# Kernel tuning notes

Hardware: AMD Instinct MI355X
Metric: run time of the kernel (lower is better)

The kernel has to match this reference:

```python
import jax, jax.numpy as jnp
import numpy as np

NUM_HEADS = 8
HEAD_DIM = 64
D_MODEL = NUM_HEADS * HEAD_DIM  # 512
B, T = 4, 2048


def setup_inputs() -> dict:
    key = jax.random.key(0)
    k1, k2 = jax.random.split(key)
    x = jax.random.normal(k1, (B, T, D_MODEL), dtype=jnp.float32)
    mask = jnp.ones((B, 1, T, T), dtype=jnp.float32)
    W = jax.random.normal(k2, (D_MODEL, 3 * D_MODEL), dtype=jnp.float32) * (D_MODEL ** -0.5)
    b = jnp.zeros((3 * D_MODEL,), dtype=jnp.float32)
    return {"x": x, "mask": mask, "W": W, "b": b}


def reference(x, mask, W, b):
    batch = x.shape[0]
    # fused QKV projection: [B, T, 3D]
    qkv = jnp.einsum("btd,de->bte", x, W) + b
    # NOTE: faithful to torch reshape [B, T, H, Hd, 3] -> the size-3 axis is innermost
    qkv = qkv.reshape(batch, -1, NUM_HEADS, HEAD_DIM, 3)
    qkv = jnp.transpose(qkv, (4, 0, 2, 1, 3))  # [3, B, H, T, Hd]
    q, k, v = qkv[0], qkv[1], qkv[2]
    logits = jnp.einsum("bhqd,bhkd->bhqk", q, k) / (HEAD_DIM ** 0.5)
    logits = logits + (1.0 - mask) * -10000.0
    w = jax.nn.softmax(logits, axis=-1)
    out = jnp.einsum("bhqk,bhkd->bhqd", w, v)  # [B, H, T, Hd]
    out = jnp.transpose(out, (0, 2, 1, 3)).reshape(batch, -1, NUM_HEADS * HEAD_DIM)
    return out
```

## Files before the change

kernel.cpp:

```cpp
#include <hip/hip_runtime.h>
#include <hip/hip_bf16.h>
#include <stdint.h>

#define B_   4
#define T_   2048
#define H_   8
#define HD_  64
#define DM_  512
#define N3_  1536

typedef short bf_el;
typedef __attribute__((ext_vector_type(8))) bf_el bfrag;
typedef __attribute__((ext_vector_type(4))) bf_el bhalf4;
typedef __attribute__((ext_vector_type(4))) float ffrag;

#define SCALE_L2E  0.18033688011112043f
#define MASK_L2E   14426.950408889634f

static __device__ __forceinline__ unsigned short f2bf(float f) {
    union { float f; unsigned int i; } v; v.f = f;
    unsigned int r = v.i + 0x7fff + ((v.i >> 16) & 1);
    return (unsigned short)(r >> 16);
}
static __device__ __forceinline__ unsigned short f2bf_fast(float f) {
    union { float f; unsigned int i; } v; v.f = f;
    return (unsigned short)((v.i + 0x8000u) >> 16);
}

static __device__ __forceinline__ unsigned int cvt_pk_bf16(float a, float b) {
    unsigned int r;
    asm("v_cvt_pk_bf16_f32 %0, %1, %2" : "=v"(r) : "v"(a), "v"(b));
    return r;
}

__global__ __launch_bounds__(256) void k_prep(const float* __restrict__ W,
                                              const float* __restrict__ X,
                                              const float* __restrict__ mask,
                                              unsigned short* __restrict__ Wt,
                                              unsigned short* __restrict__ Xb,
                                              int* __restrict__ flags) {
    __shared__ __align__(16) unsigned short Ls[64 * 72];
    const int bid = blockIdx.x;
    const int tid = threadIdx.x;

    if (bid < 512) {
        const int R0 = bid * 16;
        const int mb = R0 >> 11;
        const int q0 = R0 & 2047;
        const int e  = mb * 32 + (q0 >> 6);
        const int wave = tid >> 6, lane = tid & 63;
        unsigned int acc = 0u;
        const float* base = mask + (size_t)R0 * T_ + tid * 8;
#pragma unroll
        for (int rr = 0; rr < 16; ++rr) {
            const uint4 u0 = *(const uint4*)(base + (size_t)rr * T_);
            const uint4 u1 = *(const uint4*)(base + (size_t)rr * T_ + 4);
            acc |= (u0.x ^ 0x3F800000u) | (u0.y ^ 0x3F800000u) |
                   (u0.z ^ 0x3F800000u) | (u0.w ^ 0x3F800000u) |
                   (u1.x ^ 0x3F800000u) | (u1.y ^ 0x3F800000u) |
                   (u1.z ^ 0x3F800000u) | (u1.w ^ 0x3F800000u);
        }
        unsigned long long bal = __ballot(acc != 0u);
        if (lane == 0 && bal != 0ULL) {
#pragma unroll
            for (int j = 0; j < 8; ++j)
                if ((bal >> (8 * j)) & 0xFFULL)
                    atomicOr(&flags[e * 32 + wave * 8 + j], 1);
        }
        return;
    }
    if (bid < 768) {
        const int b2 = bid - 512;
        const float* src = X + (size_t)b2 * 16384;
        unsigned short* dst = Xb + (size_t)b2 * 16384;
#pragma unroll
        for (int j = 0; j < 8; ++j) {
            int idx = j * 512 + tid * 2;
            float4 f0 = *(const float4*)(src + idx * 4);
            float4 f1 = *(const float4*)(src + idx * 4 + 4);
            __align__(16) unsigned short t8[8];
            t8[0] = f2bf_fast(f0.x); t8[1] = f2bf_fast(f0.y);
            t8[2] = f2bf_fast(f0.z); t8[3] = f2bf_fast(f0.w);
            t8[4] = f2bf_fast(f1.x); t8[5] = f2bf_fast(f1.y);
            t8[6] = f2bf_fast(f1.z); t8[7] = f2bf_fast(f1.w);
            *(uint4*)(dst + idx * 4) = *(const uint4*)t8;
        }
        return;
    }
    {
        const int t  = bid - 768;
        const int n0 = (t % 24) * 64;
        const int k0 = (t / 24) * 64;
#pragma unroll
        for (int i = 0; i < 4; ++i) {
            int chunk = tid + i * 256;
            int k = chunk >> 4;
            int c = chunk & 15;
            float4 f = *(const float4*)(W + (size_t)(k0 + k) * N3_ + n0 + c * 4);
            unsigned short* p = Ls + k * 72 + c * 4;
            p[0] = f2bf(f.x); p[1] = f2bf(f.y); p[2] = f2bf(f.z); p[3] = f2bf(f.w);
        }
        __syncthreads();
        const int n = tid >> 2;
        const int g = tid & 3;
        __align__(16) unsigned short tmp[16];
#pragma unroll
        for (int i = 0; i < 16; ++i) tmp[i] = Ls[(g * 16 + i) * 72 + n];
        uint4* dst = (uint4*)(Wt + (size_t)(n0 + n) * DM_ + k0 + g * 16);
        dst[0] = *(const uint4*)(tmp);
        dst[1] = *(const uint4*)(tmp + 8);
    }
}

__global__ __launch_bounds__(256) void k_gemm_qkv(const unsigned short* __restrict__ Xb,
                                                  const unsigned short* __restrict__ Wt,
                                                  const float* __restrict__ bias,
                                                  unsigned short* __restrict__ Qb,
                                                  unsigned short* __restrict__ Kb,
                                                  unsigned short* __restrict__ Vtb) {
    __shared__ __align__(16) unsigned short SH[12800];
    unsigned short* As = SH;
    unsigned short* Bs = SH + 5120;
    unsigned short* Cs = SH;

    const int tid  = threadIdx.x;
    const int wave = tid >> 6;
    const int lane = tid & 63;
    const int quad = lane >> 4;
    const int l16  = lane & 15;
    const int wm = wave >> 1, wn = wave & 1;
    const int h  = blockIdx.x >> 6;
    const int m0 = (blockIdx.x & 63) * 128;
    const int n0 = h * 192;

    float bvv[6];
#pragma unroll
    for (int ni = 0; ni < 6; ++ni) bvv[ni] = bias[n0 + wn * 96 + ni * 16 + l16];

    ffrag acc[4][6];
#pragma unroll
    for (int i = 0; i < 4; ++i)
#pragma unroll
        for (int j = 0; j < 6; ++j) acc[i][j] = (ffrag){0.f, 0.f, 0.f, 0.f};

    for (int kt = 0; kt < 16; ++kt) {
        __syncthreads();
#pragma unroll
        for (int i = 0; i < 2; ++i) {
            int chunk = tid + i * 256;
            int r = chunk >> 2, c = chunk & 3;
            *(uint4*)(As + r * 40 + c * 8) =
                *(const uint4*)(Xb + (size_t)(m0 + r) * DM_ + kt * 32 + c * 8);
        }
#pragma unroll
        for (int i = 0; i < 3; ++i) {
            int chunk = tid + i * 256;
            int r = chunk >> 2, c = chunk & 3;
            *(uint4*)(Bs + r * 40 + c * 8) =
                *(const uint4*)(Wt + (size_t)(n0 + r) * DM_ + kt * 32 + c * 8);
        }
        __syncthreads();
        bfrag af[4], bfr[6];
#pragma unroll
        for (int mi = 0; mi < 4; ++mi)
            af[mi] = *(const bfrag*)(As + (wm * 64 + mi * 16 + l16) * 40 + quad * 8);
#pragma unroll
        for (int ni = 0; ni < 6; ++ni)
            bfr[ni] = *(const bfrag*)(Bs + (wn * 96 + ni * 16 + l16) * 40 + quad * 8);
#pragma unroll
        for (int mi = 0; mi < 4; ++mi)
#pragma unroll
            for (int ni = 0; ni < 6; ++ni)
                acc[mi][ni] = __builtin_amdgcn_mfma_f32_16x16x32_bf16(af[mi], bfr[ni], acc[mi][ni], 0, 0, 0);
    }

    const int b   = m0 >> 11;
    const int tb0 = m0 & 2047;
    const size_t bh = (size_t)(b * 8 + h);
    float cscale[6];
#pragma unroll
    for (int ni = 0; ni < 6; ++ni) {
        int c = wn * 96 + ni * 16 + l16;
        cscale[ni] = (c % 3 == 0) ? SCALE_L2E : 1.0f;
    }
#pragma unroll
    for (int half = 0; half < 2; ++half) {
        __syncthreads();
        if (wm == half) {
#pragma unroll
            for (int mi = 0; mi < 4; ++mi)
#pragma unroll
                for (int ni = 0; ni < 6; ++ni)
#pragma unroll
                    for (int reg = 0; reg < 4; ++reg) {
                        int r = mi * 16 + quad * 4 + reg;
                        int c = wn * 96 + ni * 16 + l16;
                        Cs[r * 200 + c] = f2bf_fast((acc[mi][ni][reg] + bvv[ni]) * cscale[ni]);
                    }
        }
        __syncthreads();
        const int tb = tb0 + half * 64;
#pragma unroll
        for (int i = 0; i < 2; ++i) {
            int idx = tid + i * 256;
            int tl = idx >> 3, hc = (idx & 7) * 8;
            __align__(16) unsigned short tq[8], tk[8];
#pragma unroll
            for (int j = 0; j < 8; ++j) {
                tq[j] = Cs[tl * 200 + (hc + j) * 3 + 0];
                tk[j] = Cs[tl * 200 + (hc + j) * 3 + 1];
            }
            *(uint4*)(Qb + (bh * T_ + tb + tl) * HD_ + hc) = *(const uint4*)tq;
            *(uint4*)(Kb + (bh * T_ + tb + tl) * HD_ + hc) = *(const uint4*)tk;
        }
#pragma unroll
        for (int i = 0; i < 2; ++i) {
            int idx = tid + i * 256;
            int hd = idx >> 3, t8 = (idx & 7) * 8;
            __align__(16) unsigned short tv[8];
#pragma unroll
            for (int j = 0; j < 8; ++j)
                tv[j] = Cs[(t8 + j) * 200 + hd * 3 + 2];
            *(uint4*)(Vtb + (bh * HD_ + hd) * T_ + tb + t8) = *(const uint4*)tv;
        }
    }
}

__global__ __launch_bounds__(256, 2) void k_attn(const unsigned short* __restrict__ Q,
                                                 const unsigned short* __restrict__ K,
                                                 const unsigned short* __restrict__ Vt,
                                                 const float* __restrict__ mask,
                                                 const int* __restrict__ flags,
                                                 float* __restrict__ out) {
    __shared__ __align__(16) unsigned short KVs[4][64 * 72];
    __shared__ float Rs[256];

    const int tid = threadIdx.x;
    const int wave = tid >> 6, lane = tid & 63;
    const int quad = lane >> 4, l16 = lane & 15;
    const int rg = wave & 1;
    const int kh = wave >> 1;
    const int bh = blockIdx.x & 31, b = bh >> 3, h = bh & 7;
    const int qt = blockIdx.x >> 5;
    const int q0 = qt * 128;

    bfrag qf[4][2];
#pragma unroll
    for (int g = 0; g < 4; ++g) {
        size_t qrow = ((size_t)bh * T_ + q0 + rg * 64 + g * 16 + l16) * HD_;
        qf[g][0] = *(const bfrag*)(Q + qrow + quad * 8);
        qf[g][1] = *(const bfrag*)(Q + qrow + 32 + quad * 8);
    }
    float lsum[4] = {0.f, 0.f, 0.f, 0.f};
    ffrag of[4][4];
#pragma unroll
    for (int g = 0; g < 4; ++g)
#pragma unroll
        for (int nb = 0; nb < 4; ++nb) of[g][nb] = (ffrag){0.f, 0.f, 0.f, 0.f};

    const int fbase = (b * 32 + qt * 2 + rg) * 32;

    const int sr0 = tid >> 3, sr1 = (tid + 256) >> 3, sc = tid & 7;
    const unsigned short* Kbase = K  + (size_t)bh * T_ * HD_;
    const unsigned short* Vbase = Vt + (size_t)bh * HD_ * T_;

    uint4 kreg[2], vreg[2];
    kreg[0] = *(const uint4*)(Kbase + (size_t)sr0 * HD_ + sc * 8);
    kreg[1] = *(const uint4*)(Kbase + (size_t)sr1 * HD_ + sc * 8);
    vreg[0] = *(const uint4*)(Vbase + (size_t)sr0 * T_ + sc * 8);
    vreg[1] = *(const uint4*)(Vbase + (size_t)sr1 * T_ + sc * 8);
    *(uint4*)(&KVs[0][sr0 * 72 + sc * 8]) = kreg[0];
    *(uint4*)(&KVs[0][sr1 * 72 + sc * 8]) = kreg[1];
    *(uint4*)(&KVs[2][sr0 * 72 + sc * 8]) = vreg[0];
    *(uint4*)(&KVs[2][sr1 * 72 + sc * 8]) = vreg[1];
    __syncthreads();

    for (int kt = 0; kt < 32; ++kt) {
        const int cur = kt & 1;
        if (kt < 31) {
            const int kn = (kt + 1) * 64;
            kreg[0] = *(const uint4*)(Kbase + (size_t)(kn + sr0) * HD_ + sc * 8);
            kreg[1] = *(const uint4*)(Kbase + (size_t)(kn + sr1) * HD_ + sc * 8);
            vreg[0] = *(const uint4*)(Vbase + (size_t)sr0 * T_ + kn + sc * 8);
            vreg[1] = *(const uint4*)(Vbase + (size_t)sr1 * T_ + kn + sc * 8);
        }
        const int fl = flags[fbase + kt];

        bfrag kf[2][2];
#pragma unroll
        for (int ns = 0; ns < 2; ++ns) {
            const int nsg = kh * 2 + ns;
#pragma unroll
            for (int ks = 0; ks < 2; ++ks)
                kf[ns][ks] = *(const bfrag*)(&KVs[cur][(nsg * 16 + l16) * 72 + (ks * 4 + quad) * 8]);
        }
        bfrag vfr[4];
#pragma unroll
        for (int nb = 0; nb < 4; ++nb) {
            union { bhalf4 h[2]; bfrag f; } vv;
            vv.h[0] = *(const bhalf4*)(&KVs[2 + cur][(nb * 16 + l16) * 72 + kh * 32 + quad * 4]);
            vv.h[1] = *(const bhalf4*)(&KVs[2 + cur][(nb * 16 + l16) * 72 + kh * 32 + 16 + quad * 4]);
            vfr[nb] = vv.f;
        }

#pragma unroll
        for (int g = 0; g < 4; ++g) {
            ffrag st[2];
#pragma unroll
            for (int ns = 0; ns < 2; ++ns) {
                ffrag a = (ffrag){0.f, 0.f, 0.f, 0.f};
                a = __builtin_amdgcn_mfma_f32_16x16x32_bf16(kf[ns][0], qf[g][0], a, 0, 0, 0);
                a = __builtin_amdgcn_mfma_f32_16x16x32_bf16(kf[ns][1], qf[g][1], a, 0, 0, 0);
                st[ns] = a;
            }
            float p[2][4];
            if (fl) {
                const float* mrow = mask + ((size_t)b * T_ + q0 + rg * 64 + g * 16 + l16) * T_
                                  + kt * 64 + kh * 32 + quad * 4;
#pragma unroll
                for (int ns = 0; ns < 2; ++ns) {
                    float mv[4];
                    *(float4*)mv = *(const float4*)(mrow + ns * 16);
#pragma unroll
                    for (int reg = 0; reg < 4; ++reg) {
                        float pv = __builtin_amdgcn_exp2f(
                            fmaf(mv[reg], MASK_L2E, st[ns][reg] - MASK_L2E));
                        p[ns][reg] = pv;
                        lsum[g] += pv;
                    }
                }
            } else {
#pragma unroll
                for (int ns = 0; ns < 2; ++ns)
#pragma unroll
                    for (int reg = 0; reg < 4; ++reg) {
                        float pv = __builtin_amdgcn_exp2f(st[ns][reg]);
                        p[ns][reg] = pv;
                        lsum[g] += pv;
                    }
            }
            union { unsigned int u[4]; bfrag s; } pa;
            pa.u[0] = cvt_pk_bf16(p[0][0], p[0][1]);
            pa.u[1] = cvt_pk_bf16(p[0][2], p[0][3]);
            pa.u[2] = cvt_pk_bf16(p[1][0], p[1][1]);
            pa.u[3] = cvt_pk_bf16(p[1][2], p[1][3]);
#pragma unroll
            for (int nb = 0; nb < 4; ++nb)
                of[g][nb] = __builtin_amdgcn_mfma_f32_16x16x32_bf16(pa.s, vfr[nb], of[g][nb], 0, 0, 0);
        }
        if (kt < 31) {
            const int nxt = cur ^ 1;
            *(uint4*)(&KVs[nxt][sr0 * 72 + sc * 8]) = kreg[0];
            *(uint4*)(&KVs[nxt][sr1 * 72 + sc * 8]) = kreg[1];
            *(uint4*)(&KVs[2 + nxt][sr0 * 72 + sc * 8]) = vreg[0];
            *(uint4*)(&KVs[2 + nxt][sr1 * 72 + sc * 8]) = vreg[1];
            __syncthreads();
        }
    }

    float rsw[4];
#pragma unroll
    for (int g = 0; g < 4; ++g) {
        float r = lsum[g];
        r += __shfl_xor(r, 16, 64);
        r += __shfl_xor(r, 32, 64);
        rsw[g] = r;
    }
    __syncthreads();
    float* Fp = (float*)(&KVs[0][0]);
    if (quad == 0) {
#pragma unroll
        for (int g = 0; g < 4; ++g)
            Rs[kh * 128 + rg * 64 + g * 16 + l16] = rsw[g];
    }
    if (kh == 1) {
        float* basep = Fp + rg * (64 * 66);
#pragma unroll
        for (int g = 0; g < 4; ++g)
#pragma unroll
            for (int nb = 0; nb < 4; ++nb)
#pragma unroll
                for (int reg = 0; reg < 4; ++reg)
                    basep[(g * 16 + quad * 4 + reg) * 66 + nb * 16 + l16] = of[g][nb][reg];
    }
    __syncthreads();
    if (kh == 0) {
        const float* basep = Fp + rg * (64 * 66);
#pragma unroll
        for (int g = 0; g < 4; ++g) {
            float inv[4];
#pragma unroll
            for (int reg = 0; reg < 4; ++reg) {
                int row = rg * 64 + g * 16 + quad * 4 + reg;
                inv[reg] = 1.0f / (Rs[row] + Rs[128 + row]);
            }
#pragma unroll
            for (int nb = 0; nb < 4; ++nb)
#pragma unroll
                for (int reg = 0; reg < 4; ++reg) {
                    float v = of[g][nb][reg] + basep[(g * 16 + quad * 4 + reg) * 66 + nb * 16 + l16];
                    int t = q0 + rg * 64 + g * 16 + quad * 4 + reg;
                    out[((size_t)b * T_ + t) * DM_ + h * 64 + nb * 16 + l16] = v * inv[reg];
                }
        }
    }
}

extern "C" void kernel_launch(void* const* d_in, const int* in_sizes, int n_in,
                              void* d_out, int out_size, void* d_ws, size_t ws_size,
                              hipStream_t stream) {
    const float* X    = (const float*)d_in[0];
    const float* mask = (const float*)d_in[1];
    const float* W    = (const float*)d_in[2];
    const float* bias = (const float*)d_in[3];
    float* outp = (float*)d_out;

    char* ws = (char*)d_ws;
    unsigned short* Wt  = (unsigned short*)(ws);
    unsigned short* Xb  = (unsigned short*)(ws + 1572864);
    unsigned short* Qb  = (unsigned short*)(ws + 9961472);
    unsigned short* Kb  = (unsigned short*)(ws + 18350080);
    unsigned short* Vtb = (unsigned short*)(ws + 26738688);
    int*            flg = (int*)(ws + 35127296);

    hipMemsetAsync(flg, 0, 16384, stream);
    k_prep     <<<dim3(960), 256, 0, stream>>>(W, X, mask, Wt, Xb, flg);
    k_gemm_qkv <<<dim3(512), 256, 0, stream>>>(Xb, Wt, bias, Qb, Kb, Vtb);
    k_attn     <<<dim3(512), 256, 0, stream>>>(Qb, Kb, Vtb, mask, flg, outp);
}
```

Before: 197.7 us.

## Load K/V fragments directly from global into registers and pack mask flags into bitmasks

The attention kernel drops the LDS double-buffered K/V staging and its per-tile barriers. Each wave now loads its MFMA K and V fragments straight from global memory into registers, ping-ponging two register sets so the next tile's loads overlap the current tile's compute. Mask-nonuniform flags are packed into one 32-bit word per query group, set with a single atomicOr, which shrinks the memset and the per-tile flag loads. The risk is uncoalesced, redundant global and L2 reads, since every wave refetches K/V that the LDS path shared. Holding two fragment sets also raises register pressure.

Result: slower. 246.2 us (+24.5%).

```diff
diff --git a/kernel.cpp b/kernel.cpp
--- a/kernel.cpp
+++ b/kernel.cpp
@@ -62,10 +62,12 @@
         }
         unsigned long long bal = __ballot(acc != 0u);
         if (lane == 0 && bal != 0ULL) {
+            unsigned int bits = 0u;
 #pragma unroll
             for (int j = 0; j < 8; ++j)
                 if ((bal >> (8 * j)) & 0xFFULL)
-                    atomicOr(&flags[e * 32 + wave * 8 + j], 1);
+                    bits |= (1u << (wave * 8 + j));
+            atomicOr((unsigned int*)&flags[e], bits);
         }
         return;
     }
@@ -232,7 +234,7 @@
                                                  const float* __restrict__ mask,
                                                  const int* __restrict__ flags,
                                                  float* __restrict__ out) {
-    __shared__ __align__(16) unsigned short KVs[4][64 * 72];
+    __shared__ float Fp[2][64 * 66];
     __shared__ float Rs[256];
 
     const int tid = threadIdx.x;
@@ -258,51 +260,30 @@
 #pragma unroll
         for (int nb = 0; nb < 4; ++nb) of[g][nb] = (ffrag){0.f, 0.f, 0.f, 0.f};
 
-    const int fbase = (b * 32 + qt * 2 + rg) * 32;
-
-    const int sr0 = tid >> 3, sr1 = (tid + 256) >> 3, sc = tid & 7;
-    const unsigned short* Kbase = K  + (size_t)bh * T_ * HD_;
-    const unsigned short* Vbase = Vt + (size_t)bh * HD_ * T_;
-
-    uint4 kreg[2], vreg[2];
-    kreg[0] = *(const uint4*)(Kbase + (size_t)sr0 * HD_ + sc * 8);
-    kreg[1] = *(const uint4*)(Kbase + (size_t)sr1 * HD_ + sc * 8);
-    vreg[0] = *(const uint4*)(Vbase + (size_t)sr0 * T_ + sc * 8);
-    vreg[1] = *(const uint4*)(Vbase + (size_t)sr1 * T_ + sc * 8);
-    *(uint4*)(&KVs[0][sr0 * 72 + sc * 8]) = kreg[0];
-    *(uint4*)(&KVs[0][sr1 * 72 + sc * 8]) = kreg[1];
-    *(uint4*)(&KVs[2][sr0 * 72 + sc * 8]) = vreg[0];
-    *(uint4*)(&KVs[2][sr1 * 72 + sc * 8]) = vreg[1];
-    __syncthreads();
-
-    for (int kt = 0; kt < 32; ++kt) {
-        const int cur = kt & 1;
-        if (kt < 31) {
-            const int kn = (kt + 1) * 64;
-            kreg[0] = *(const uint4*)(Kbase + (size_t)(kn + sr0) * HD_ + sc * 8);
-            kreg[1] = *(const uint4*)(Kbase + (size_t)(kn + sr1) * HD_ + sc * 8);
-            vreg[0] = *(const uint4*)(Vbase + (size_t)sr0 * T_ + kn + sc * 8);
-            vreg[1] = *(const uint4*)(Vbase + (size_t)sr1 * T_ + kn + sc * 8);
-        }
-        const int fl = flags[fbase + kt];
-
-        bfrag kf[2][2];
-#pragma unroll
-        for (int ns = 0; ns < 2; ++ns) {
-            const int nsg = kh * 2 + ns;
+    const unsigned int flbits = ((const unsigned int*)flags)[b * 32 + qt * 2 + rg];
+
+    const unsigned short* Kp = K  + (size_t)bh * T_ * HD_ + (kh * 32 + l16) * HD_ + quad * 8;
+    const unsigned short* Vp = Vt + (size_t)bh * HD_ * T_ + (size_t)l16 * T_ + kh * 32 + quad * 4;
+
+    auto loadK = [&](bfrag (&kf)[2][2], int kt) {
+        const unsigned short* p = Kp + kt * (64 * HD_);
+#pragma unroll
+        for (int ns = 0; ns < 2; ++ns)
 #pragma unroll
             for (int ks = 0; ks < 2; ++ks)
-                kf[ns][ks] = *(const bfrag*)(&KVs[cur][(nsg * 16 + l16) * 72 + (ks * 4 + quad) * 8]);
-        }
-        bfrag vfr[4];
-#pragma unroll
-        for (int nb = 0; nb < 4; ++nb) {
-            union { bhalf4 h[2]; bfrag f; } vv;
-            vv.h[0] = *(const bhalf4*)(&KVs[2 + cur][(nb * 16 + l16) * 72 + kh * 32 + quad * 4]);
-            vv.h[1] = *(const bhalf4*)(&KVs[2 + cur][(nb * 16 + l16) * 72 + kh * 32 + 16 + quad * 4]);
-            vfr[nb] = vv.f;
-        }
-
+                kf[ns][ks] = *(const bfrag*)(p + ns * (16 * HD_) + ks * 32);
+    };
+    auto loadV = [&](bhalf4 (&vf)[2][4], int kt) {
+        const unsigned short* p = Vp + kt * 64;
+#pragma unroll
+        for (int nb = 0; nb < 4; ++nb)
+#pragma unroll
+            for (int ns = 0; ns < 2; ++ns)
+                vf[ns][nb] = *(const bhalf4*)(p + (size_t)nb * (16 * T_) + ns * 16);
+    };
+
+    auto compute = [&](const bfrag (&kf)[2][2], const bhalf4 (&vf)[2][4], int kt) {
+        const int fl = (int)((flbits >> kt) & 1u);
 #pragma unroll
         for (int g = 0; g < 4; ++g) {
             ffrag st[2];
@@ -345,17 +326,24 @@
             pa.u[2] = cvt_pk_bf16(p[1][0], p[1][1]);
             pa.u[3] = cvt_pk_bf16(p[1][2], p[1][3]);
 #pragma unroll
-            for (int nb = 0; nb < 4; ++nb)
-                of[g][nb] = __builtin_amdgcn_mfma_f32_16x16x32_bf16(pa.s, vfr[nb], of[g][nb], 0, 0, 0);
-        }
-        if (kt < 31) {
-            const int nxt = cur ^ 1;
-            *(uint4*)(&KVs[nxt][sr0 * 72 + sc * 8]) = kreg[0];
-            *(uint4*)(&KVs[nxt][sr1 * 72 + sc * 8]) = kreg[1];
-            *(uint4*)(&KVs[2 + nxt][sr0 * 72 + sc * 8]) = vreg[0];
-            *(uint4*)(&KVs[2 + nxt][sr1 * 72 + sc * 8]) = vreg[1];
-            __syncthreads();
-        }
+            for (int nb = 0; nb < 4; ++nb) {
+                union { bhalf4 h[2]; bfrag f; } vv;
+                vv.h[0] = vf[0][nb];
+                vv.h[1] = vf[1][nb];
+                of[g][nb] = __builtin_amdgcn_mfma_f32_16x16x32_bf16(pa.s, vv.f, of[g][nb], 0, 0, 0);
+            }
+        }
+    };
+
+    bfrag  kfA[2][2], kfB[2][2];
+    bhalf4 vfA[2][4], vfB[2][4];
+    loadK(kfA, 0); loadV(vfA, 0);
+    for (int kt2 = 0; kt2 < 16; ++kt2) {
+        const int kt = kt2 * 2;
+        loadK(kfB, kt + 1); loadV(vfB, kt + 1);
+        compute(kfA, vfA, kt);
+        if (kt2 < 15) { loadK(kfA, kt + 2); loadV(vfA, kt + 2); }
+        compute(kfB, vfB, kt + 1);
     }
 
     float rsw[4];
@@ -367,14 +355,13 @@
         rsw[g] = r;
     }
     __syncthreads();
-    float* Fp = (float*)(&KVs[0][0]);
     if (quad == 0) {
 #pragma unroll
         for (int g = 0; g < 4; ++g)
             Rs[kh * 128 + rg * 64 + g * 16 + l16] = rsw[g];
     }
     if (kh == 1) {
-        float* basep = Fp + rg * (64 * 66);
+        float* basep = &Fp[rg][0];
 #pragma unroll
         for (int g = 0; g < 4; ++g)
 #pragma unroll
@@ -385,7 +372,7 @@
     }
     __syncthreads();
     if (kh == 0) {
-        const float* basep = Fp + rg * (64 * 66);
+        const float* basep = &Fp[rg][0];
 #pragma unroll
         for (int g = 0; g < 4; ++g) {
             float inv[4];
@@ -423,7 +410,7 @@
     unsigned short* Vtb = (unsigned short*)(ws + 26738688);
     int*            flg = (int*)(ws + 35127296);
 
-    hipMemsetAsync(flg, 0, 16384, stream);
+    hipMemsetAsync(flg, 0, 512, stream);
     k_prep     <<<dim3(960), 256, 0, stream>>>(W, X, mask, Wt, Xb, flg);
     k_gemm_qkv <<<dim3(512), 256, 0, stream>>>(Xb, Wt, bias, Qb, Kb, Vtb);
     k_attn     <<<dim3(512), 256, 0, stream>>>(Qb, Kb, Vtb, mask, flg, outp);
```
